# Performance work log

Measured on AMD Instinct MI355X. Metric: run time of the kernel, lower is better.

The kernel has to match this reference:

```python
import jax, jax.numpy as jnp
import numpy as np
import math

H = 2048; NH = 16; HD = 128; E = 8; K = 2; F = 8192; CAP_F = 1.25
B = 2; S = 2048

def _layernorm(x, scale, bias, eps=1e-5):
    m = jnp.mean(x, axis=-1, keepdims=True)
    v = jnp.var(x, axis=-1, keepdims=True)
    return (x - m) * jax.lax.rsqrt(v + eps) * scale + bias

def _rope(x):
    # x: [B, S, NH, HD]; half-split RoPE, theta=10000
    hd = x.shape[-1]
    pos = jnp.arange(x.shape[1], dtype=jnp.float32)
    freqs = 1.0 / (10000.0 ** (jnp.arange(0, hd // 2, dtype=jnp.float32) / (hd // 2)))
    ang = pos[:, None] * freqs[None, :]              # [S, HD/2]
    cos = jnp.cos(ang)[None, :, None, :]
    sin = jnp.sin(ang)[None, :, None, :]
    x1, x2 = jnp.split(x, 2, axis=-1)
    return jnp.concatenate([x1 * cos - x2 * sin, x1 * sin + x2 * cos], axis=-1)

def setup_inputs() -> dict:
    key = jax.random.key(0)
    ks = jax.random.split(key, 16)
    std = 0.02
    inp = {
        'hidden_states': jax.random.normal(ks[0], (B, S, H), jnp.float32),
        'attention_mask': jnp.ones((B, S), jnp.int32),
        'ln1_scale': jnp.ones((H,), jnp.float32), 'ln1_bias': jnp.zeros((H,), jnp.float32),
        'ln2_scale': jnp.ones((H,), jnp.float32), 'ln2_bias': jnp.zeros((H,), jnp.float32),
        'Wq': jax.random.normal(ks[1], (H, NH * HD), jnp.float32) * std,
        'Wk': jax.random.normal(ks[2], (H, NH * HD), jnp.float32) * std,
        'Wv': jax.random.normal(ks[3], (H, NH * HD), jnp.float32) * std,
        'Wo': jax.random.normal(ks[4], (NH * HD, H), jnp.float32) * std,
        'Wg': jax.random.normal(ks[5], (H, H), jnp.float32) * std,
        'bg': jnp.zeros((H,), jnp.float32),
        'ls_attn': jnp.full((H,), 0.1, jnp.float32),
        'ls_moe': jnp.full((H,), 0.1, jnp.float32),
        'router_w': jax.random.normal(ks[6], (H, E), jnp.float32) * std,
        'W1': jax.random.normal(ks[7], (E, H, F), jnp.float32) * std,
        'b1': jnp.zeros((E, F), jnp.float32),
        'W2': jax.random.normal(ks[8], (E, F, H), jnp.float32) * std,
        'b2': jnp.zeros((E, H), jnp.float32),
    }
    return inp

def _forward(hidden_states, attention_mask, ln1_scale, ln1_bias, ln2_scale, ln2_bias,
             Wq, Wk, Wv, Wo, Wg, bg, ls_attn, ls_moe, router_w, W1, b1, W2, b2):
    b, s, h = hidden_states.shape
    # ---- pre-norm MLA attention + residual ----
    xn = _layernorm(hidden_states, ln1_scale, ln1_bias)
    q = (xn @ Wq).reshape(b, s, NH, HD)
    k = (xn @ Wk).reshape(b, s, NH, HD)
    v = (xn @ Wv).reshape(b, s, NH, HD)
    q = _rope(q); k = _rope(k)
    scores = jnp.einsum('bqhd,bkhd->bhqk', q, k) / math.sqrt(HD)
    causal = jnp.tril(jnp.ones((s, s), bool))
    mask = causal[None, None, :, :] & (attention_mask[:, None, None, :] > 0)
    scores = jnp.where(mask, scores, -1e9)
    attn = jax.nn.softmax(scores, axis=-1)
    ctx = jnp.einsum('bhqk,bkhd->bqhd', attn, v).reshape(b, s, NH * HD)
    attn_out = ctx @ Wo
    attn_out = attn_out * jax.nn.sigmoid(xn @ Wg + bg)   # output gating
    attn_out = attn_out * ls_attn                         # layer scale
    hidden_states = hidden_states + attn_out
    # ---- pre-norm MoE FFN + residual ----
    xn2 = _layernorm(hidden_states, ln2_scale, ln2_bias)
    T = b * s
    x = xn2.reshape(T, h)
    logits = (x @ router_w).astype(jnp.float32)           # [T, E]
    probs = jax.nn.softmax(logits, axis=-1)
    gates, idx = jax.lax.top_k(probs, K)                  # [T, K]
    gates = gates / jnp.sum(gates, axis=-1, keepdims=True)
    cap = int(math.ceil(T * K / E * CAP_F))               # expert capacity
    e_flat = idx.reshape(T * K)
    g_flat = gates.reshape(T * K)
    oh = jax.nn.one_hot(e_flat, E, dtype=jnp.int32)       # [TK, E]
    pos = jnp.sum(jnp.cumsum(oh, axis=0) * oh, axis=-1) - 1
    keep = (pos < cap).astype(x.dtype)
    pos_c = jnp.clip(pos, 0, cap - 1)
    x_rep = jnp.repeat(x, K, axis=0)                      # [TK, H]
    buf = jnp.zeros((E, cap, h), x.dtype).at[e_flat, pos_c].add(x_rep * keep[:, None])
    hmid = jax.nn.gelu(jnp.einsum('ech,ehf->ecf', buf, W1) + b1[:, None, :])
    obuf = jnp.einsum('ecf,efh->ech', hmid, W2) + b2[:, None, :]
    tok = obuf[e_flat, pos_c] * (keep * g_flat)[:, None]  # [TK, H]
    moe_out = tok.reshape(T, K, h).sum(axis=1).reshape(b, s, h)
    moe_out = moe_out * ls_moe
    return hidden_states + moe_out

def reference(hidden_states, attention_mask, ln1_scale, ln1_bias, ln2_scale, ln2_bias,
              Wq, Wk, Wv, Wo, Wg, bg, ls_attn, ls_moe, router_w, W1, b1, W2, b2):
    return _forward(hidden_states, attention_mask, ln1_scale, ln1_bias, ln2_scale, ln2_bias,
                    Wq, Wk, Wv, Wo, Wg, bg, ls_attn, ls_moe, router_w, W1, b1, W2, b2)
```

## Files before the change

### kernel.cpp

```cpp
#include <hip/hip_runtime.h>
#include <hip/hip_fp16.h>

typedef _Float16 f16;
typedef _Float16 half8 __attribute__((ext_vector_type(8)));
typedef float floatx4 __attribute__((ext_vector_type(4)));

constexpr int kH  = 2048;
constexpr int kS  = 2048;
constexpr int kB  = 2;
constexpr int kT  = kB * kS;
constexpr int kNH = 16;
constexpr int kHD = 128;
constexpr int kE  = 8;
constexpr int kF  = 8192;
constexpr int kCAP = 1280;
constexpr int kTK = kT * 2;

__device__ __forceinline__ void gload16(const void* g, void* lds_) {
  __builtin_amdgcn_global_load_lds((const __attribute__((address_space(1))) void*)g,
                                   (__attribute__((address_space(3))) void*)lds_,
                                   16, 0, 0);
}

__device__ __forceinline__ void xcd_remap(int& bx, int& by, int& bz) {
  const int gx = gridDim.x, gy = gridDim.y;
  const int nwg = gx * gy * gridDim.z;
  int L = (bz * gy + by) * gx + bx;
  L = (L & 7) * (nwg >> 3) + (L >> 3);
  bz = L / (gx * gy);
  const int r = L - bz * gx * gy;
  by = r / gx;  bx = r - by * gx;
}

__global__ __launch_bounds__(256) void transpose_cvt(
    const float* __restrict__ src, f16* __restrict__ dst,
    int ldS, int ldD, long sZ, long dZ)
{
  __shared__ float tile[64][65];
  src += (long)blockIdx.z * sZ;
  dst += (long)blockIdx.z * dZ;
  const int kb = blockIdx.y * 64, nb = blockIdx.x * 64;
  const int tx = threadIdx.x & 15, ty = threadIdx.x >> 4;
#pragma unroll
  for (int i = 0; i < 4; i++) {
    const int r = ty + i * 16;
    const float4 v = *(const float4*)&src[(long)(kb + r) * ldS + nb + tx * 4];
    tile[r][tx * 4 + 0] = v.x; tile[r][tx * 4 + 1] = v.y;
    tile[r][tx * 4 + 2] = v.z; tile[r][tx * 4 + 3] = v.w;
  }
  __syncthreads();
#pragma unroll
  for (int i = 0; i < 4; i++) {
    const int n = ty + i * 16;
    union { f16 h[4]; unsigned long long u; } pk;
#pragma unroll
    for (int j = 0; j < 4; j++) pk.h[j] = (f16)tile[tx * 4 + j][n];
    *(unsigned long long*)&dst[(long)(nb + n) * ldD + kb + tx * 4] = pk.u;
  }
}

__global__ __launch_bounds__(256) void ln_kernel(
    const float* __restrict__ x, const float* __restrict__ sc,
    const float* __restrict__ bi, f16* __restrict__ o16, float* __restrict__ o32)
{
  const long row = blockIdx.x;
  const float* xr = x + row * kH;
  const int t = threadIdx.x;
  const float4 u = ((const float4*)xr)[t * 2];
  const float4 v = ((const float4*)xr)[t * 2 + 1];
  float s = u.x + u.y + u.z + u.w + v.x + v.y + v.z + v.w;
  float q = u.x*u.x + u.y*u.y + u.z*u.z + u.w*u.w + v.x*v.x + v.y*v.y + v.z*v.z + v.w*v.w;
#pragma unroll
  for (int m = 1; m < 64; m <<= 1) { s += __shfl_xor(s, m); q += __shfl_xor(q, m); }
  __shared__ float red_s[4], red_q[4];
  const int w = t >> 6, l = t & 63;
  if (l == 0) { red_s[w] = s; red_q[w] = q; }
  __syncthreads();
  s = red_s[0] + red_s[1] + red_s[2] + red_s[3];
  q = red_q[0] + red_q[1] + red_q[2] + red_q[3];
  const float mean = s * (1.f / kH);
  const float var = q * (1.f / kH) - mean * mean;
  const float rstd = rsqrtf(var + 1e-5f);
  const int c = t * 8;
  const float vals[8] = {u.x, u.y, u.z, u.w, v.x, v.y, v.z, v.w};
#pragma unroll
  for (int j = 0; j < 8; j++) {
    const float y = (vals[j] - mean) * rstd * sc[c + j] + bi[c + j];
    o16[row * kH + c + j] = (f16)y;
    if (o32 != nullptr) o32[row * kH + c + j] = y;
  }
}

template <int EPI>
__global__ __launch_bounds__(256) void gemm_kernel(
    const f16* __restrict__ A, const f16* __restrict__ B, void* __restrict__ Cv,
    const float* __restrict__ bias, const int* __restrict__ rowCount,
    int M, int N, int K, long aZ, long bZ, long cZ, long biasZ)
{
  const int z = blockIdx.z;
  if (rowCount != nullptr && (int)(blockIdx.y * 128) >= rowCount[z]) return;
  __shared__ f16 As[128 * 64];
  __shared__ f16 Bs[128 * 64];
  A += (long)z * aZ;  B += (long)z * bZ;
  const int tid = threadIdx.x, w = tid >> 6, l = tid & 63;
  const int g = l >> 4, lr = l & 15;
  const long m0 = (long)blockIdx.y * 128, n0 = (long)blockIdx.x * 128;
  const int wm = (w >> 1) * 64, wn = (w & 1) * 64;
  floatx4 acc[4][4];
#pragma unroll
  for (int i = 0; i < 4; i++)
#pragma unroll
    for (int j = 0; j < 4; j++) acc[i][j] = floatx4{0.f, 0.f, 0.f, 0.f};
  const int lrow = l >> 3, lwb = (l & 7) * 16;
  const int nk = K >> 6;
  for (int kt = 0; kt < nk; kt++) {
    const long k0 = (long)kt * 64;
#pragma unroll
    for (int c = 0; c < 4; c++) {
      const int rbase = w * 32 + c * 8;
      const int row = rbase + lrow;
      const int srcoff = (lwb ^ ((row & 7) << 4)) >> 1;
      gload16(A + (m0 + row) * K + k0 + srcoff, As + rbase * 64);
      gload16(B + (n0 + row) * K + k0 + srcoff, Bs + rbase * 64);
    }
    asm volatile("s_waitcnt vmcnt(0)" ::: "memory");
    __syncthreads();
#pragma unroll
    for (int kc = 0; kc < 2; kc++) {
      half8 af[4], bf[4];
#pragma unroll
      for (int i = 0; i < 4; i++) {
        const int ra = wm + i * 16 + lr;
        af[i] = *(const half8*)((const char*)As + ra * 128 + ((kc * 64 + g * 16) ^ ((ra & 7) << 4)));
        const int rb = wn + i * 16 + lr;
        bf[i] = *(const half8*)((const char*)Bs + rb * 128 + ((kc * 64 + g * 16) ^ ((rb & 7) << 4)));
      }
#pragma unroll
      for (int mi = 0; mi < 4; mi++)
#pragma unroll
        for (int ni = 0; ni < 4; ni++)
          acc[mi][ni] = __builtin_amdgcn_mfma_f32_16x16x32_f16(af[mi], bf[ni], acc[mi][ni], 0, 0, 0);
    }
    __syncthreads();
  }
  const long crow = m0 + wm + g * 4;
  const long ccol = n0 + wn + lr;
#pragma unroll
  for (int mi = 0; mi < 4; mi++)
#pragma unroll
    for (int ni = 0; ni < 4; ni++)
#pragma unroll
      for (int j = 0; j < 4; j++) {
        const long r = crow + mi * 16 + j;
        const long c = ccol + ni * 16;
        float v = acc[mi][ni][j];
        if (EPI == 0) {
          ((float*)Cv)[(long)z * cZ + r * N + c] = v;
        } else {
          v += bias[(long)z * biasZ + c];
          ((f16*)Cv)[(long)z * cZ + r * N + c] = (f16)v;
        }
      }
}

#define STG(SRC, TILE, KC, PAR, MAT) { \
  const f16* s_ = (SRC) + (long)(TILE) * 64 + (KC) * 32; \
  char* d_ = lds + ((PAR) * 65536 + (MAT) * 32768 + (KC) * 16384) + ldsW; \
  gload16(s_, d_); \
  gload16(s_ + 128 * ldGl, d_ + 8192); }

#define MROW(MH, MM, AF) \
  acc[(MH)*4+(MM)][0] = __builtin_amdgcn_mfma_f32_16x16x32_f16(AF, bf0, acc[(MH)*4+(MM)][0], 0, 0, 0); \
  acc[(MH)*4+(MM)][1] = __builtin_amdgcn_mfma_f32_16x16x32_f16(AF, bf1, acc[(MH)*4+(MM)][1], 0, 0, 0); \
  acc[(MH)*4+(MM)][2] = __builtin_amdgcn_mfma_f32_16x16x32_f16(AF, bf2, acc[(MH)*4+(MM)][2], 0, 0, 0); \
  acc[(MH)*4+(MM)][3] = __builtin_amdgcn_mfma_f32_16x16x32_f16(AF, bf3, acc[(MH)*4+(MM)][3], 0, 0, 0);

#define PH(PAR, KC, MH, RB, STAGE_STMT, VM_STMT) { \
  const char* au_ = lds + ((PAR) * 65536 + (KC) * 16384); \
  const char* bu_ = lds + ((PAR) * 65536 + 32768 + (KC) * 16384); \
  af0 = *(const half8*)(au_ + afoff + (MH) * 4096 +    0); \
  af1 = *(const half8*)(au_ + afoff + (MH) * 4096 + 1024); \
  af2 = *(const half8*)(au_ + afoff + (MH) * 4096 + 2048); \
  af3 = *(const half8*)(au_ + afoff + (MH) * 4096 + 3072); \
  if (RB) { \
    bf0 = *(const half8*)(bu_ + bfoff +    0); \
    bf1 = *(const half8*)(bu_ + bfoff + 1024); \
    bf2 = *(const half8*)(bu_ + bfoff + 2048); \
    bf3 = *(const half8*)(bu_ + bfoff + 3072); \
  } \
  STAGE_STMT; \
  VM_STMT; \
  __builtin_amdgcn_sched_barrier(0); \
  __builtin_amdgcn_s_barrier(); \
  asm volatile("s_waitcnt lgkmcnt(0)" ::: "memory"); \
  __builtin_amdgcn_sched_barrier(0); \
  __builtin_amdgcn_s_setprio(1); \
  MROW(MH, 0, af0) MROW(MH, 1, af1) MROW(MH, 2, af2) MROW(MH, 3, af3) \
  __builtin_amdgcn_s_setprio(0); }

#define VM10 asm volatile("s_waitcnt vmcnt(10)" ::: "memory")
#define VM8  asm volatile("s_waitcnt vmcnt(8)" ::: "memory")
#define VM4  asm volatile("s_waitcnt vmcnt(4)" ::: "memory")
#define VM0  asm volatile("s_waitcnt vmcnt(0)" ::: "memory")
#define NOP (void)0

template <int EPI, bool SPLITK>
__global__ __launch_bounds__(512, 2) void gemm8p_kernel(
    const f16* __restrict__ A, const f16* __restrict__ B, void* __restrict__ Cv,
    const float* __restrict__ bias, const int* __restrict__ rowCount,
    int M, int N, int K, long ldA, long ldB, long aZ, long bZ, long cZ,
    long cZ2, long biasZ)
{
  int bx = blockIdx.x, by = blockIdx.y, bz = blockIdx.z;
  xcd_remap(bx, by, bz);
  const int z = bz;
  const int ze = SPLITK ? (z >> 1) : z;
  if (rowCount != nullptr && (int)(by * 256) >= rowCount[ze]) return;
  __shared__ __align__(16) char lds[131072];
  const long khoff = SPLITK ? (long)(z & 1) * K : 0;
  A += (long)ze * aZ + khoff;  B += (long)ze * bZ + khoff;
  const int tid = threadIdx.x, w = tid >> 6, l = tid & 63;
  const int g = l >> 4, lr = l & 15;
  const long m0 = (long)by * 256, n0 = (long)bx * 256;
  const int wm = (w >> 2) * 128, wn = (w & 3) * 64;

  floatx4 acc[8][4];
#pragma unroll
  for (int i = 0; i < 8; i++)
#pragma unroll
    for (int j = 0; j < 4; j++) acc[i][j] = floatx4{0.f, 0.f, 0.f, 0.f};

  const int swzS = ((l & 3) * 8) ^ (((l >> 3) & 3) << 3);
  const f16* aSrc;
  const f16* bSrc;
  long ldGl;
  {
    const int srow = w * 16 + (l >> 2);
    aSrc = A + (m0 + srow) * ldA + swzS;
    bSrc = B + (n0 + srow) * ldB + swzS;
  }
  ldGl = ldA;
  const int ldsW = w * 1024;
  const int rsw = (g * 16) ^ (((lr >> 1) & 3) << 4);
  const int afoff = wm * 64 + lr * 64 + rsw;
  const int bfoff = wn * 64 + lr * 64 + rsw;
  half8 af0, af1, af2, af3;
  half8 bf0 = half8{0}, bf1 = half8{0}, bf2 = half8{0}, bf3 = half8{0};

  STG(aSrc, 0, 0, 0, 0);
  STG(bSrc, 0, 0, 0, 1);
  STG(aSrc, 0, 1, 0, 0);
  STG(bSrc, 0, 1, 0, 1);
  STG(bSrc, 1, 0, 1, 1);
  STG(aSrc, 1, 0, 1, 0);
  STG(bSrc, 1, 1, 1, 1);
  VM10;
  __builtin_amdgcn_sched_barrier(0);
  __builtin_amdgcn_s_barrier();

  const int NI = K >> 7;
  for (int i = 0; i < NI - 1; i++) {
    const int t0 = 2 * i, t1 = 2 * i + 1;
    PH(0, 0, 0, 1, STG(aSrc, (t1),     1, 1, 0), VM10)
    PH(0, 0, 1, 0, STG(bSrc, (t0 + 2), 0, 0, 1), VM10)
    PH(0, 1, 0, 1, STG(aSrc, (t0 + 2), 0, 0, 0), VM10)
    PH(0, 1, 1, 0, STG(bSrc, (t0 + 2), 1, 0, 1), VM10)
    PH(1, 0, 0, 1, STG(aSrc, (t0 + 2), 1, 0, 0), VM10)
    PH(1, 0, 1, 0, STG(bSrc, (t1 + 2), 0, 1, 1), VM10)
    PH(1, 1, 0, 1, STG(aSrc, (t1 + 2), 0, 1, 0), VM10)
    PH(1, 1, 1, 0, STG(bSrc, (t1 + 2), 1, 1, 1), VM10)
  }
  {
    const int t1 = 2 * (NI - 1) + 1;
    PH(0, 0, 0, 1, STG(aSrc, (t1), 1, 1, 0), VM8)
    PH(0, 0, 1, 0, NOP, NOP)
    PH(0, 1, 0, 1, NOP, VM4)
    PH(0, 1, 1, 0, NOP, NOP)
    PH(1, 0, 0, 1, NOP, VM0)
    PH(1, 0, 1, 0, NOP, NOP)
    PH(1, 1, 0, 1, NOP, NOP)
    PH(1, 1, 1, 0, NOP, NOP)
  }

  const long crow = m0 + wm + g * 4;
  const long ccol = n0 + wn + lr;
  float* c32 = (float*)Cv + (long)ze * cZ + (SPLITK ? (long)(z & 1) * cZ2 : 0);
#pragma unroll
  for (int mi = 0; mi < 8; mi++)
#pragma unroll
    for (int ni = 0; ni < 4; ni++)
#pragma unroll
      for (int j = 0; j < 4; j++) {
        const long r = crow + mi * 16 + j;
        const long c = ccol + ni * 16;
        float v = acc[mi][ni][j];
        if (EPI == 0) {
          c32[r * N + c] = v;
        } else if (EPI == 2) {
          v += bias[(long)ze * biasZ + c];
          const float u2 = 1.5957691216057308f * (v + 0.044715f * v * v * v);
          const float sg = 1.f / (1.f + __expf(-u2));
          ((f16*)Cv)[(long)ze * cZ + r * N + c] = (f16)(v * sg);
        } else {
          v += bias[(long)ze * biasZ + c];
          ((f16*)Cv)[(long)ze * cZ + r * N + c] = (f16)v;
        }
      }
}
#undef STG
#undef MROW
#undef PH
#undef VM10
#undef VM8
#undef VM4
#undef VM0
#undef NOP

__global__ void rope_table_kernel(float* __restrict__ ct, float* __restrict__ st) {
  const int i = blockIdx.x * 256 + threadIdx.x;
  if (i >= kS * 64) return;
  const int s = i >> 6, f = i & 63;
  const double freq = exp(-0.14391156831212787 * (double)f);
  const double ang = (double)s * freq;
  ct[i] = (float)cos(ang);
  st[i] = (float)sin(ang);
}

__global__ __launch_bounds__(256) void rope_kernel(
    const float* __restrict__ q, const float* __restrict__ k,
    const float* __restrict__ ct, const float* __restrict__ st,
    f16* __restrict__ qr, f16* __restrict__ kr)
{
  const long t = blockIdx.x;
  const int s = (int)(t & (kS - 1)), b = (int)(t >> 11);
  for (int u = threadIdx.x; u < kNH * 64; u += 256) {
    const int h = u >> 6, i = u & 63;
    const float c = ct[s * 64 + i], sn = st[s * 64 + i];
    const long src = t * kH + h * kHD + i;
    const long dst = (((long)(b * kNH + h)) * kS + s) * kHD + i;
    float x1 = q[src], x2 = q[src + 64];
    qr[dst]      = (f16)((x1 * c - x2 * sn) * 0.08838834764831845f);
    qr[dst + 64] = (f16)((x1 * sn + x2 * c) * 0.08838834764831845f);
    x1 = k[src]; x2 = k[src + 64];
    kr[dst]      = (f16)(x1 * c - x2 * sn);
    kr[dst + 64] = (f16)(x1 * sn + x2 * c);
  }
}

__global__ __launch_bounds__(256) void attn_kernel(
    const f16* __restrict__ q_r, const f16* __restrict__ k_r,
    const f16* __restrict__ v_t, f16* __restrict__ ctx)
{
  __shared__ f16 Ks[64 * 128];
  __shared__ f16 Vs[128 * 64];
  __shared__ f16 Ps[4][1024];
  int qt = blockIdx.x, h = blockIdx.y, b = blockIdx.z;
  xcd_remap(qt, h, b);
  const int bh = b * kNH + h;
  const int tid = threadIdx.x, w = tid >> 6, l = tid & 63;
  const int g = l >> 4, lr = l & 15;
  const long q0 = (long)qt * 64;
  const f16* qbase = q_r + ((long)bh * kS + q0 + w * 16 + lr) * kHD;
  half8 qf[4];
#pragma unroll
  for (int kc = 0; kc < 4; kc++) qf[kc] = *(const half8*)(qbase + kc * 32 + g * 8);
  floatx4 acc[8];
#pragma unroll
  for (int i = 0; i < 8; i++) acc[i] = floatx4{0.f, 0.f, 0.f, 0.f};
  float mrun[4], lrun[4];
#pragma unroll
  for (int j = 0; j < 4; j++) { mrun[j] = -1e30f; lrun[j] = 0.f; }
  f16* pw = Ps[w];

  for (int kt = 0; kt <= qt; kt++) {
    const long k0 = (long)kt * 64;
#pragma unroll
    for (int c = 0; c < 4; c++) {
      const int cc = w * 4 + c;
      const int row = cc * 4 + (l >> 4);
      const int wb = (l & 15) * 16;
      const int src = (wb ^ ((row & 7) << 4)) >> 1;
      gload16(k_r + ((long)bh * kS + k0 + row) * kHD + src, Ks + cc * 512);
    }
#pragma unroll
    for (int c = 0; c < 4; c++) {
      const int cc = w * 4 + c;
      const int row = cc * 8 + (l >> 3);
      const int wb = (l & 7) * 16;
      const int src = (wb ^ ((row & 7) << 4)) >> 1;
      gload16(v_t + ((long)bh * kHD + row) * kS + k0 + src, Vs + cc * 512);
    }
    asm volatile("s_waitcnt vmcnt(0)" ::: "memory");
    __syncthreads();

    floatx4 sfr[4];
#pragma unroll
    for (int f = 0; f < 4; f++) {
      floatx4 s4 = floatx4{0.f, 0.f, 0.f, 0.f};
      const int row = f * 16 + lr;
#pragma unroll
      for (int kc = 0; kc < 4; kc++) {
        const half8 kfq = *(const half8*)((const char*)Ks + row * 256 +
                            ((kc * 64 + g * 16) ^ ((row & 7) << 4)));
        s4 = __builtin_amdgcn_mfma_f32_16x16x32_f16(qf[kc], kfq, s4, 0, 0, 0);
      }
      sfr[f] = s4;
    }
    if (kt == qt) {
#pragma unroll
      for (int f = 0; f < 4; f++) {
        const int key = kt * 64 + f * 16 + lr;
#pragma unroll
        for (int j = 0; j < 4; j++) {
          const int qrow = qt * 64 + w * 16 + g * 4 + j;
          if (key > qrow) sfr[f][j] = -1e30f;
        }
      }
    }
    float al[4];
#pragma unroll
    for (int j = 0; j < 4; j++) {
      float pm = fmaxf(fmaxf(sfr[0][j], sfr[1][j]), fmaxf(sfr[2][j], sfr[3][j]));
      pm = fmaxf(pm, __shfl_xor(pm, 1)); pm = fmaxf(pm, __shfl_xor(pm, 2));
      pm = fmaxf(pm, __shfl_xor(pm, 4)); pm = fmaxf(pm, __shfl_xor(pm, 8));
      const float mn = fmaxf(mrun[j], pm);
      al[j] = __expf(mrun[j] - mn);
      mrun[j] = mn;
      float rs = 0.f;
#pragma unroll
      for (int f = 0; f < 4; f++) {
        const float p = __expf(sfr[f][j] - mn);
        sfr[f][j] = p; rs += p;
      }
      rs += __shfl_xor(rs, 1); rs += __shfl_xor(rs, 2);
      rs += __shfl_xor(rs, 4); rs += __shfl_xor(rs, 8);
      lrun[j] = lrun[j] * al[j] + rs;
    }
#pragma unroll
    for (int nf = 0; nf < 8; nf++)
#pragma unroll
      for (int j = 0; j < 4; j++) acc[nf][j] *= al[j];
#pragma unroll
    for (int f = 0; f < 4; f++)
#pragma unroll
      for (int j = 0; j < 4; j++) {
        const int row = g * 4 + j;
        const int byteoff = (row * 128 + (f * 16 + lr) * 2) ^ ((row & 7) << 4);
        *(f16*)((char*)pw + byteoff) = (f16)sfr[f][j];
      }
#pragma unroll
    for (int kc = 0; kc < 2; kc++) {
      const half8 pf = *(const half8*)((const char*)pw + lr * 128 +
                         ((kc * 64 + g * 16) ^ ((lr & 7) << 4)));
#pragma unroll
      for (int nf = 0; nf < 8; nf++) {
        const int vrow = nf * 16 + lr;
        const half8 vfr = *(const half8*)((const char*)Vs + vrow * 128 +
                            ((kc * 64 + g * 16) ^ ((vrow & 7) << 4)));
        acc[nf] = __builtin_amdgcn_mfma_f32_16x16x32_f16(pf, vfr, acc[nf], 0, 0, 0);
      }
    }
    __syncthreads();
  }
  const long orow = (long)b * kS + q0 + w * 16;
#pragma unroll
  for (int j = 0; j < 4; j++) {
    const float inv = 1.0f / lrun[j];
    const int r = g * 4 + j;
#pragma unroll
    for (int nf = 0; nf < 8; nf++)
      ctx[(orow + r) * kH + h * kHD + nf * 16 + lr] = (f16)(acc[nf][j] * inv);
  }
}

__global__ __launch_bounds__(256) void combine1_kernel(
    const float* __restrict__ hid, const float* __restrict__ alin,
    const float* __restrict__ glin, const float* __restrict__ bg,
    const float* __restrict__ ls, float* __restrict__ out)
{
  const long i = (long)blockIdx.x * 256 + threadIdx.x;
  const float4 hv = ((const float4*)hid)[i];
  const float4 av = ((const float4*)alin)[i];
  const float4 gv = ((const float4*)glin)[i];
  const int c = (int)(i & 511);
  const float4 lv = ((const float4*)ls)[c];
  const float4 bv = ((const float4*)bg)[c];
  float4 o;
  o.x = hv.x + lv.x * av.x / (1.f + __expf(-(gv.x + bv.x)));
  o.y = hv.y + lv.y * av.y / (1.f + __expf(-(gv.y + bv.y)));
  o.z = hv.z + lv.z * av.z / (1.f + __expf(-(gv.z + bv.z)));
  o.w = hv.w + lv.w * av.w / (1.f + __expf(-(gv.w + bv.w)));
  ((float4*)out)[i] = o;
}

__global__ __launch_bounds__(256) void router_kernel(
    const float* __restrict__ x, const float* __restrict__ rw,
    int* __restrict__ eidx, float* __restrict__ gates)
{
  const int t = blockIdx.x * 4 + (threadIdx.x >> 6);
  const int l = threadIdx.x & 63;
  const float* xr = x + (long)t * kH;
  float a[8] = {0.f, 0.f, 0.f, 0.f, 0.f, 0.f, 0.f, 0.f};
  for (int it = 0; it < kH / 64; it++) {
    const float xv = xr[it * 64 + l];
    const float* r = rw + (long)(it * 64 + l) * kE;
#pragma unroll
    for (int e = 0; e < 8; e++) a[e] += xv * r[e];
  }
#pragma unroll
  for (int e = 0; e < 8; e++)
#pragma unroll
    for (int m = 1; m < 64; m <<= 1) a[e] += __shfl_xor(a[e], m);
  if (l == 0) {
    float mx = a[0];
#pragma unroll
    for (int e = 1; e < 8; e++) mx = fmaxf(mx, a[e]);
    float p[8];
#pragma unroll
    for (int e = 0; e < 8; e++) p[e] = __expf(a[e] - mx);
    int i1 = 0; float v1 = p[0];
#pragma unroll
    for (int e = 1; e < 8; e++) if (p[e] > v1) { v1 = p[e]; i1 = e; }
    int i2 = -1; float v2 = -1.f;
#pragma unroll
    for (int e = 0; e < 8; e++) if (e != i1 && p[e] > v2) { v2 = p[e]; i2 = e; }
    const float inv = 1.f / (v1 + v2);
    eidx[t * 2] = i1; eidx[t * 2 + 1] = i2;
    gates[t * 2] = v1 * inv; gates[t * 2 + 1] = v2 * inv;
  }
}

__global__ void scan_kernel(const int* __restrict__ eidx, int* __restrict__ slot,
                            int* __restrict__ counts)
{
  const int l = threadIdx.x;
  int base[8] = {0, 0, 0, 0, 0, 0, 0, 0};
  const unsigned long long lt = (1ull << l) - 1ull;
  for (int it = 0; it < kTK / 64; it++) {
    const int i = it * 64 + l;
    const int e = eidx[i];
    int mypos = 0;
#pragma unroll
    for (int ex = 0; ex < 8; ex++) {
      const unsigned long long mk = __ballot(e == ex);
      if (e == ex) mypos = base[ex] + __popcll(mk & lt);
      base[ex] += __popcll(mk);
    }
    slot[i] = (mypos < kCAP) ? e * kCAP + mypos : -1;
  }
  if (l == 0) {
#pragma unroll
    for (int ex = 0; ex < 8; ex++) counts[ex] = min(base[ex], kCAP);
  }
}

__global__ __launch_bounds__(256) void scatter_kernel(
    const f16* __restrict__ xh, const int* __restrict__ slot, f16* __restrict__ buf)
{
  const int i = blockIdx.x;
  const int s = slot[i];
  if (s < 0) return;
  const long t = i >> 1;
  ((half8*)(buf + (long)s * kH))[threadIdx.x] =
      ((const half8*)(xh + t * kH))[threadIdx.x];
}

__global__ __launch_bounds__(256) void combine2_kernel(
    const float* __restrict__ hid2, const float* __restrict__ P0,
    const float* __restrict__ P1, const int* __restrict__ slot,
    const float* __restrict__ gates, const float* __restrict__ b2,
    const float* __restrict__ ls, float* __restrict__ out)
{
  const int t = blockIdx.x;
  const int c = threadIdx.x * 8;
  float m[8] = {0.f, 0.f, 0.f, 0.f, 0.f, 0.f, 0.f, 0.f};
#pragma unroll
  for (int ks = 0; ks < 2; ks++) {
    const int s = slot[t * 2 + ks];
    if (s < 0) continue;
    const float gte = gates[t * 2 + ks];
    const int e = s / kCAP;
    const long ro = (long)s * kH + c;
    const float4 p0a = *(const float4*)&P0[ro];
    const float4 p0b = *(const float4*)&P0[ro + 4];
    const float4 p1a = *(const float4*)&P1[ro];
    const float4 p1b = *(const float4*)&P1[ro + 4];
    const float4 ba = *(const float4*)&b2[e * kH + c];
    const float4 bb = *(const float4*)&b2[e * kH + c + 4];
    m[0] += gte * (p0a.x + p1a.x + ba.x);
    m[1] += gte * (p0a.y + p1a.y + ba.y);
    m[2] += gte * (p0a.z + p1a.z + ba.z);
    m[3] += gte * (p0a.w + p1a.w + ba.w);
    m[4] += gte * (p0b.x + p1b.x + bb.x);
    m[5] += gte * (p0b.y + p1b.y + bb.y);
    m[6] += gte * (p0b.z + p1b.z + bb.z);
    m[7] += gte * (p0b.w + p1b.w + bb.w);
  }
  const float* hp = hid2 + (long)t * kH + c;
  float* op = out + (long)t * kH + c;
#pragma unroll
  for (int j = 0; j < 8; j++) op[j] = hp[j] + ls[c + j] * m[j];
}

extern "C" void kernel_launch(void* const* d_in, const int* in_sizes, int n_in,
                              void* d_out, int out_size, void* d_ws, size_t ws_size,
                              hipStream_t stream)
{
  (void)in_sizes; (void)n_in;
  const float* hidden   = (const float*)d_in[0];
  const float* ln1s     = (const float*)d_in[2];
  const float* ln1b     = (const float*)d_in[3];
  const float* ln2s     = (const float*)d_in[4];
  const float* ln2b     = (const float*)d_in[5];
  const float* Wq       = (const float*)d_in[6];
  const float* Wk       = (const float*)d_in[7];
  const float* Wv       = (const float*)d_in[8];
  const float* Wo       = (const float*)d_in[9];
  const float* Wg       = (const float*)d_in[10];
  const float* bg       = (const float*)d_in[11];
  const float* ls_attn  = (const float*)d_in[12];
  const float* ls_moe   = (const float*)d_in[13];
  const float* router_w = (const float*)d_in[14];
  const float* W1       = (const float*)d_in[15];
  const float* b1       = (const float*)d_in[16];
  const float* W2       = (const float*)d_in[17];
  const float* b2       = (const float*)d_in[18];

  char* ws = (char*)d_ws;
  size_t off = 0;
  auto take = [&](size_t b) { size_t r = off; off += (b + 255) & ~(size_t)255; return r; };
  const size_t o_wT   = take(5ULL * kH * kH * 2);
  const size_t o_w1t  = take((size_t)kE * kF * kH * 2);
  const size_t o_w2t  = take((size_t)kE * kH * kF * 2);
  const size_t o_xn   = take((size_t)kT * kH * 2);
  const size_t o_qkvg = take(4ULL * kT * kH * 4);
  const size_t o_tab  = take(2ULL * kS * 64 * 4);
  const size_t o_qr   = take(3ULL * kT * kH * 2);
  const size_t o_ctx  = take((size_t)kT * kH * 2);
  const size_t o_h2   = take((size_t)kT * kH * 4);
  const size_t o_sm   = take(1 << 20);
  const size_t o_hmid = take((size_t)kE * kCAP * kF * 2);
  if (off > ws_size) { hipMemsetAsync(d_out, 0xFF, (size_t)out_size * 4, stream); return; }

  f16* wT    = (f16*)(ws + o_wT);
  f16* w1t   = (f16*)(ws + o_w1t);
  f16* w2t   = (f16*)(ws + o_w2t);
  f16* xn    = (f16*)(ws + o_xn);
  float* qf  = (float*)(ws + o_qkvg);
  float* kfp = qf + (size_t)kT * kH;
  float* vfp = kfp + (size_t)kT * kH;
  float* gfp = vfp + (size_t)kT * kH;
  float* tabc = (float*)(ws + o_tab);
  float* tabs = tabc + (size_t)kS * 64;
  f16* qr  = (f16*)(ws + o_qr);
  f16* kr  = qr + (size_t)kT * kH;
  f16* vt  = kr + (size_t)kT * kH;
  f16* ctx = (f16*)(ws + o_ctx);
  float* h2 = (float*)(ws + o_h2);
  int* eidx    = (int*)(ws + o_sm);
  float* gates = (float*)(ws + o_sm + 65536);
  int* slot    = (int*)(ws + o_sm + 131072);
  int* counts  = (int*)(ws + o_sm + 196608);
  f16* hmid = (f16*)(ws + o_hmid);
  float* attn_lin = qf;
  float* x2f = vfp;
  f16* x2h  = (f16*)(ws + o_qkvg + 1ULL * kT * kH * 4 + (size_t)kT * kH * 2);
  f16* buf  = qr;
  float* P0 = (float*)(ws + o_qkvg);
  float* P1 = (float*)(ws + o_w1t);
  const long pStride = (long)(P1 - P0);

  const long HH = (long)kH * kH;

  transpose_cvt<<<dim3(32, 32, 1), 256, 0, stream>>>(Wq, wT + 0 * HH, kH, kH, 0, 0);
  transpose_cvt<<<dim3(32, 32, 1), 256, 0, stream>>>(Wk, wT + 1 * HH, kH, kH, 0, 0);
  transpose_cvt<<<dim3(32, 32, 1), 256, 0, stream>>>(Wv, wT + 2 * HH, kH, kH, 0, 0);
  transpose_cvt<<<dim3(32, 32, 1), 256, 0, stream>>>(Wg, wT + 3 * HH, kH, kH, 0, 0);
  transpose_cvt<<<dim3(32, 32, 1), 256, 0, stream>>>(Wo, wT + 4 * HH, kH, kH, 0, 0);
  transpose_cvt<<<dim3(kF / 64, kH / 64, kE), 256, 0, stream>>>(
      W1, w1t, kF, kH, (long)kH * kF, (long)kF * kH);
  transpose_cvt<<<dim3(kH / 64, kF / 64, kE), 256, 0, stream>>>(
      W2, w2t, kH, kF, (long)kF * kH, (long)kH * kF);
  ln_kernel<<<kT, 256, 0, stream>>>(hidden, ln1s, ln1b, xn, nullptr);
  gemm8p_kernel<0, false><<<dim3(kH / 256, kT / 256, 4), 512, 0, stream>>>(
      xn, wT, qf, nullptr, nullptr, kT, kH, kH, kH, kH,
      0L, HH, (long)kT * kH, 0L, 0L);
  rope_table_kernel<<<(kS * 64 + 255) / 256, 256, 0, stream>>>(tabc, tabs);
  rope_kernel<<<kT, 256, 0, stream>>>(qf, kfp, tabc, tabs, qr, kr);
  for (int b = 0; b < kB; b++)
    transpose_cvt<<<dim3(kHD / 64, kS / 64, kNH), 256, 0, stream>>>(
        vfp + (size_t)b * kS * kH, vt + (size_t)b * kNH * kHD * kS,
        kH, kS, 128L, (long)kHD * kS);
  attn_kernel<<<dim3(kS / 64, kNH, kB), 256, 0, stream>>>(qr, kr, vt, ctx);
  gemm_kernel<0><<<dim3(kH / 128, kT / 128, 1), 256, 0, stream>>>(
      ctx, wT + 4 * HH, attn_lin, nullptr, nullptr, kT, kH, kH, 0L, 0L, 0L, 0L);
  combine1_kernel<<<(kT * kH / 4) / 256, 256, 0, stream>>>(
      hidden, attn_lin, gfp, bg, ls_attn, h2);
  ln_kernel<<<kT, 256, 0, stream>>>(h2, ln2s, ln2b, x2h, x2f);
  router_kernel<<<kT / 4, 256, 0, stream>>>(x2f, router_w, eidx, gates);
  scan_kernel<<<1, 64, 0, stream>>>(eidx, slot, counts);
  scatter_kernel<<<kTK, 256, 0, stream>>>(x2h, slot, buf);
  gemm8p_kernel<2, false><<<dim3(kF / 256, kCAP / 256, kE), 512, 0, stream>>>(
      buf, w1t, hmid, b1, counts, kCAP, kF, kH, kH, kH,
      (long)kCAP * kH, (long)kF * kH, (long)kCAP * kF, 0L, (long)kF);
  gemm8p_kernel<0, true><<<dim3(kH / 256, kCAP / 256, 2 * kE), 512, 0, stream>>>(
      hmid, w2t, P0, nullptr, counts, kCAP, kH, 4096, kF, kF,
      (long)kCAP * kF, (long)kH * kF, (long)kCAP * kH, pStride, 0L);
  combine2_kernel<<<kT, 256, 0, stream>>>(
      h2, P0, P1, slot, gates, b2, ls_moe, (float*)d_out);
}
```

Before: 1.635 ms.

## Run Wo projection on pipelined 256x256 GEMM with split-K and make XCD remap optional

The output projection moves off the simple 128x128 GEMM onto the pipelined 256-tile kernel. K is split in two, the partial sums go to two fp32 buffers, and combine1 adds them together when it applies the gate. The XCD block remap becomes a template flag, enabled for the QKVG and Wo GEMMs and disabled for the two expert GEMMs. This brings the Wo GEMM up to the faster kernel and gives it more blocks, at the cost of writing and reading an extra fp32 partial buffer.

```diff
diff --git a/kernel.cpp b/kernel.cpp
--- a/kernel.cpp
+++ b/kernel.cpp
@@ -89,78 +89,6 @@
     o16[row * kH + c + j] = (f16)y;
     if (o32 != nullptr) o32[row * kH + c + j] = y;
   }
-}
-
-template <int EPI>
-__global__ __launch_bounds__(256) void gemm_kernel(
-    const f16* __restrict__ A, const f16* __restrict__ B, void* __restrict__ Cv,
-    const float* __restrict__ bias, const int* __restrict__ rowCount,
-    int M, int N, int K, long aZ, long bZ, long cZ, long biasZ)
-{
-  const int z = blockIdx.z;
-  if (rowCount != nullptr && (int)(blockIdx.y * 128) >= rowCount[z]) return;
-  __shared__ f16 As[128 * 64];
-  __shared__ f16 Bs[128 * 64];
-  A += (long)z * aZ;  B += (long)z * bZ;
-  const int tid = threadIdx.x, w = tid >> 6, l = tid & 63;
-  const int g = l >> 4, lr = l & 15;
-  const long m0 = (long)blockIdx.y * 128, n0 = (long)blockIdx.x * 128;
-  const int wm = (w >> 1) * 64, wn = (w & 1) * 64;
-  floatx4 acc[4][4];
-#pragma unroll
-  for (int i = 0; i < 4; i++)
-#pragma unroll
-    for (int j = 0; j < 4; j++) acc[i][j] = floatx4{0.f, 0.f, 0.f, 0.f};
-  const int lrow = l >> 3, lwb = (l & 7) * 16;
-  const int nk = K >> 6;
-  for (int kt = 0; kt < nk; kt++) {
-    const long k0 = (long)kt * 64;
-#pragma unroll
-    for (int c = 0; c < 4; c++) {
-      const int rbase = w * 32 + c * 8;
-      const int row = rbase + lrow;
-      const int srcoff = (lwb ^ ((row & 7) << 4)) >> 1;
-      gload16(A + (m0 + row) * K + k0 + srcoff, As + rbase * 64);
-      gload16(B + (n0 + row) * K + k0 + srcoff, Bs + rbase * 64);
-    }
-    asm volatile("s_waitcnt vmcnt(0)" ::: "memory");
-    __syncthreads();
-#pragma unroll
-    for (int kc = 0; kc < 2; kc++) {
-      half8 af[4], bf[4];
-#pragma unroll
-      for (int i = 0; i < 4; i++) {
-        const int ra = wm + i * 16 + lr;
-        af[i] = *(const half8*)((const char*)As + ra * 128 + ((kc * 64 + g * 16) ^ ((ra & 7) << 4)));
-        const int rb = wn + i * 16 + lr;
-        bf[i] = *(const half8*)((const char*)Bs + rb * 128 + ((kc * 64 + g * 16) ^ ((rb & 7) << 4)));
-      }
-#pragma unroll
-      for (int mi = 0; mi < 4; mi++)
-#pragma unroll
-        for (int ni = 0; ni < 4; ni++)
-          acc[mi][ni] = __builtin_amdgcn_mfma_f32_16x16x32_f16(af[mi], bf[ni], acc[mi][ni], 0, 0, 0);
-    }
-    __syncthreads();
-  }
-  const long crow = m0 + wm + g * 4;
-  const long ccol = n0 + wn + lr;
-#pragma unroll
-  for (int mi = 0; mi < 4; mi++)
-#pragma unroll
-    for (int ni = 0; ni < 4; ni++)
-#pragma unroll
-      for (int j = 0; j < 4; j++) {
-        const long r = crow + mi * 16 + j;
-        const long c = ccol + ni * 16;
-        float v = acc[mi][ni][j];
-        if (EPI == 0) {
-          ((float*)Cv)[(long)z * cZ + r * N + c] = v;
-        } else {
-          v += bias[(long)z * biasZ + c];
-          ((f16*)Cv)[(long)z * cZ + r * N + c] = (f16)v;
-        }
-      }
 }
 
 #define STG(SRC, TILE, KC, PAR, MAT) { \
@@ -204,7 +132,7 @@
 #define VM0  asm volatile("s_waitcnt vmcnt(0)" ::: "memory")
 #define NOP (void)0
 
-template <int EPI, bool SPLITK>
+template <int EPI, bool SPLITK, bool XCD>
 __global__ __launch_bounds__(512, 2) void gemm8p_kernel(
     const f16* __restrict__ A, const f16* __restrict__ B, void* __restrict__ Cv,
     const float* __restrict__ bias, const int* __restrict__ rowCount,
@@ -212,7 +140,7 @@
     long cZ2, long biasZ)
 {
   int bx = blockIdx.x, by = blockIdx.y, bz = blockIdx.z;
-  xcd_remap(bx, by, bz);
+  if (XCD) xcd_remap(bx, by, bz);
   const int z = bz;
   const int ze = SPLITK ? (z >> 1) : z;
   if (rowCount != nullptr && (int)(by * 256) >= rowCount[ze]) return;
@@ -474,22 +402,24 @@
 }
 
 __global__ __launch_bounds__(256) void combine1_kernel(
-    const float* __restrict__ hid, const float* __restrict__ alin,
-    const float* __restrict__ glin, const float* __restrict__ bg,
-    const float* __restrict__ ls, float* __restrict__ out)
+    const float* __restrict__ hid, const float* __restrict__ a0,
+    const float* __restrict__ a1, const float* __restrict__ glin,
+    const float* __restrict__ bg, const float* __restrict__ ls,
+    float* __restrict__ out)
 {
   const long i = (long)blockIdx.x * 256 + threadIdx.x;
   const float4 hv = ((const float4*)hid)[i];
-  const float4 av = ((const float4*)alin)[i];
+  const float4 av = ((const float4*)a0)[i];
+  const float4 aw = ((const float4*)a1)[i];
   const float4 gv = ((const float4*)glin)[i];
   const int c = (int)(i & 511);
   const float4 lv = ((const float4*)ls)[c];
   const float4 bv = ((const float4*)bg)[c];
   float4 o;
-  o.x = hv.x + lv.x * av.x / (1.f + __expf(-(gv.x + bv.x)));
-  o.y = hv.y + lv.y * av.y / (1.f + __expf(-(gv.y + bv.y)));
-  o.z = hv.z + lv.z * av.z / (1.f + __expf(-(gv.z + bv.z)));
-  o.w = hv.w + lv.w * av.w / (1.f + __expf(-(gv.w + bv.w)));
+  o.x = hv.x + lv.x * (av.x + aw.x) / (1.f + __expf(-(gv.x + bv.x)));
+  o.y = hv.y + lv.y * (av.y + aw.y) / (1.f + __expf(-(gv.y + bv.y)));
+  o.z = hv.z + lv.z * (av.z + aw.z) / (1.f + __expf(-(gv.z + bv.z)));
+  o.w = hv.w + lv.w * (av.w + aw.w) / (1.f + __expf(-(gv.w + bv.w)));
   ((float4*)out)[i] = o;
 }
 
@@ -662,10 +592,11 @@
   int* slot    = (int*)(ws + o_sm + 131072);
   int* counts  = (int*)(ws + o_sm + 196608);
   f16* hmid = (f16*)(ws + o_hmid);
-  float* attn_lin = qf;
   float* x2f = vfp;
   f16* x2h  = (f16*)(ws + o_qkvg + 1ULL * kT * kH * 4 + (size_t)kT * kH * 2);
   f16* buf  = qr;
+  float* woP0 = qf;
+  float* woP1 = kfp;
   float* P0 = (float*)(ws + o_qkvg);
   float* P1 = (float*)(ws + o_w1t);
   const long pStride = (long)(P1 - P0);
@@ -682,7 +613,7 @@
   transpose_cvt<<<dim3(kH / 64, kF / 64, kE), 256, 0, stream>>>(
       W2, w2t, kH, kF, (long)kF * kH, (long)kH * kF);
   ln_kernel<<<kT, 256, 0, stream>>>(hidden, ln1s, ln1b, xn, nullptr);
-  gemm8p_kernel<0, false><<<dim3(kH / 256, kT / 256, 4), 512, 0, stream>>>(
+  gemm8p_kernel<0, false, true><<<dim3(kH / 256, kT / 256, 4), 512, 0, stream>>>(
       xn, wT, qf, nullptr, nullptr, kT, kH, kH, kH, kH,
       0L, HH, (long)kT * kH, 0L, 0L);
   rope_table_kernel<<<(kS * 64 + 255) / 256, 256, 0, stream>>>(tabc, tabs);
@@ -692,18 +623,19 @@
         vfp + (size_t)b * kS * kH, vt + (size_t)b * kNH * kHD * kS,
         kH, kS, 128L, (long)kHD * kS);
   attn_kernel<<<dim3(kS / 64, kNH, kB), 256, 0, stream>>>(qr, kr, vt, ctx);
-  gemm_kernel<0><<<dim3(kH / 128, kT / 128, 1), 256, 0, stream>>>(
-      ctx, wT + 4 * HH, attn_lin, nullptr, nullptr, kT, kH, kH, 0L, 0L, 0L, 0L);
+  gemm8p_kernel<0, true, true><<<dim3(kH / 256, kT / 256, 2), 512, 0, stream>>>(
+      ctx, wT + 4 * HH, woP0, nullptr, nullptr, kT, kH, 1024, kH, kH,
+      0L, 0L, 0L, (long)kT * kH, 0L);
   combine1_kernel<<<(kT * kH / 4) / 256, 256, 0, stream>>>(
-      hidden, attn_lin, gfp, bg, ls_attn, h2);
+      hidden, woP0, woP1, gfp, bg, ls_attn, h2);
   ln_kernel<<<kT, 256, 0, stream>>>(h2, ln2s, ln2b, x2h, x2f);
   router_kernel<<<kT / 4, 256, 0, stream>>>(x2f, router_w, eidx, gates);
   scan_kernel<<<1, 64, 0, stream>>>(eidx, slot, counts);
   scatter_kernel<<<kTK, 256, 0, stream>>>(x2h, slot, buf);
-  gemm8p_kernel<2, false><<<dim3(kF / 256, kCAP / 256, kE), 512, 0, stream>>>(
+  gemm8p_kernel<2, false, false><<<dim3(kF / 256, kCAP / 256, kE), 512, 0, stream>>>(
       buf, w1t, hmid, b1, counts, kCAP, kF, kH, kH, kH,
       (long)kCAP * kH, (long)kF * kH, (long)kCAP * kF, 0L, (long)kF);
-  gemm8p_kernel<0, true><<<dim3(kH / 256, kCAP / 256, 2 * kE), 512, 0, stream>>>(
+  gemm8p_kernel<0, true, false><<<dim3(kH / 256, kCAP / 256, 2 * kE), 512, 0, stream>>>(
       hmid, w2t, P0, nullptr, counts, kCAP, kH, 4096, kF, kF,
       (long)kCAP * kF, (long)kH * kF, (long)kCAP * kH, pStride, 0L);
   combine2_kernel<<<kT, 256, 0, stream>>>(
```

Result: faster. 1.566 ms (-4.2%).
